# Kernel optimization log

Measured on AMD Instinct MI355X. Metric: run time of the kernel, lower is better.

The kernel has to match this reference:

```python
import jax, jax.numpy as jnp
import numpy as np

B_, L_, D_MODEL, N_LAYER, VOCAB = 4, 2048, 512, 2, 128
D_INNER, D_STATE, DT_RANK, D_CONV = 2 * D_MODEL, 16, D_MODEL // 16, 4
NDIR = 2  # forward / backward Mamba stacks


def setup_inputs() -> dict:
    key = jax.random.key(0)
    ks = jax.random.split(key, 12)
    f = jax.random.normal
    A_init = jnp.broadcast_to(
        jnp.log(jnp.arange(1, D_STATE + 1, dtype=jnp.float32)),
        (NDIR, N_LAYER, D_INNER, D_STATE)) + 0.0
    return {
        "input_ids": jax.random.randint(ks[0], (B_, L_), 0, VOCAB),
        "padding_mask": jnp.ones((B_, L_), dtype=bool),
        "embed": 0.02 * f(ks[1], (NDIR, VOCAB, D_MODEL)),
        "in_proj_w": 0.02 * f(ks[2], (NDIR, N_LAYER, 2 * D_INNER, D_MODEL)),
        "conv_w": 0.1 * f(ks[3], (NDIR, N_LAYER, D_INNER, 1, D_CONV)),
        "conv_b": 0.1 * f(ks[4], (NDIR, N_LAYER, D_INNER)),
        "x_proj_w": 0.02 * f(ks[5], (NDIR, N_LAYER, DT_RANK + 2 * D_STATE, D_INNER)),
        "dt_proj_w": 0.1 * f(ks[6], (NDIR, N_LAYER, D_INNER, DT_RANK)),
        "dt_proj_b": -4.0 + 0.5 * jax.random.uniform(ks[7], (NDIR, N_LAYER, D_INNER)),
        "A_log": A_init,
        "D": jnp.ones((NDIR, N_LAYER, D_INNER)),
        "out_proj_w": 0.02 * f(ks[8], (NDIR, N_LAYER, D_MODEL, D_INNER)),
        "norm_w": jnp.ones((NDIR, N_LAYER, D_MODEL)),
        "norm_f_w": jnp.ones((NDIR, D_MODEL)),
        "proj_w": 0.02 * f(ks[9], (D_MODEL, 2 * D_MODEL)),
        "proj_b": jnp.zeros((D_MODEL,)),
    }


def _rmsnorm(x, w, eps=1e-5):
    return x * jax.lax.rsqrt(jnp.mean(jnp.square(x), axis=-1, keepdims=True) + eps) * w


def _selective_scan(u, dt, Bm, Cm, A, Dp):
    # u, dt: (b, l, d_inner); Bm, Cm: (b, l, d_state)
    b, l, di = u.shape

    def step(h, inp):
        u_t, dt_t, b_t, c_t = inp                      # (b,di) (b,di) (b,n) (b,n)
        dA = jnp.exp(dt_t[:, :, None] * A)             # (b, di, n)
        h = dA * h + (dt_t * u_t)[:, :, None] * b_t[:, None, :]
        return h, jnp.einsum('bdn,bn->bd', h, c_t)

    h0 = jnp.zeros((b, di, A.shape[-1]), u.dtype)
    xs = (jnp.swapaxes(u, 0, 1), jnp.swapaxes(dt, 0, 1),
          jnp.swapaxes(Bm, 0, 1), jnp.swapaxes(Cm, 0, 1))
    _, ys = jax.lax.scan(step, h0, xs)                 # ys: (l, b, di)
    return jnp.swapaxes(ys, 0, 1) + u * Dp


def _mamba(x, p):
    in_w, cw, cb, xw, dtw, dtb, alog, dp, ow = p
    xz = jnp.einsum('bld,ed->ble', x, in_w)            # (b, l, 2*d_inner)
    u, z = jnp.split(xz, 2, axis=-1)
    uc = jnp.swapaxes(u, 1, 2)                         # (b, d_inner, l)
    uc = jax.lax.conv_general_dilated(
        uc, cw, (1,), [(D_CONV - 1, 0)], feature_group_count=D_INNER)
    u = jax.nn.silu(jnp.swapaxes(uc + cb[None, :, None], 1, 2))
    xdbl = jnp.einsum('bld,ed->ble', u, xw)
    dt, Bm, Cm = jnp.split(xdbl, [DT_RANK, DT_RANK + D_STATE], axis=-1)
    dt = jax.nn.softplus(jnp.einsum('blr,dr->bld', dt, dtw) + dtb)
    y = _selective_scan(u, dt, Bm, Cm, -jnp.exp(alog), dp)
    y = y * jax.nn.silu(z)
    return jnp.einsum('bld,ed->ble', y, ow)


def _mixer(ids, d, embed, in_proj_w, conv_w, conv_b, x_proj_w, dt_proj_w,
           dt_proj_b, A_log, D, out_proj_w, norm_w, norm_f_w):
    hidden = embed[d][ids]
    residual = None
    for i in range(N_LAYER):
        residual = hidden if residual is None else hidden + residual
        hidden = _rmsnorm(residual, norm_w[d, i])
        p = (in_proj_w[d, i], conv_w[d, i], conv_b[d, i], x_proj_w[d, i],
             dt_proj_w[d, i], dt_proj_b[d, i], A_log[d, i], D[d, i],
             out_proj_w[d, i])
        hidden = _mamba(hidden, p)
    return _rmsnorm(hidden + residual, norm_f_w[d])


def reference(input_ids, padding_mask, embed, in_proj_w, conv_w, conv_b,
              x_proj_w, dt_proj_w, dt_proj_b, A_log, D, out_proj_w, norm_w,
              norm_f_w, proj_w, proj_b):
    args = (embed, in_proj_w, conv_w, conv_b, x_proj_w, dt_proj_w, dt_proj_b,
            A_log, D, out_proj_w, norm_w, norm_f_w)
    fwd = _mixer(input_ids, 0, *args)
    bwd = jnp.flip(_mixer(jnp.flip(input_ids, 1), 1, *args), 1)
    out = jnp.concatenate([fwd, bwd], axis=-1)        # (b, l, 2*d_model)
    return jnp.einsum('ble,oe->blo', out, proj_w) + proj_b
```

## Files before the change

### kernel.cpp

```cpp
#include <hip/hip_runtime.h>
#include <hip/hip_bf16.h>

#define B_   4
#define L_   2048
#define DM   512
#define DI   1024
#define NST  16
#define DTR  32
#define ROWS (B_ * L_)
#define NCHUNK 64
#define CLEN  (L_ / NCHUNK)
#define LN2R 1.4426950408889634f

typedef unsigned short u16;
typedef __attribute__((ext_vector_type(8))) short bf16x8;
typedef __attribute__((ext_vector_type(4))) float f32x4;
typedef __attribute__((ext_vector_type(4))) float float4v;
typedef __attribute__((ext_vector_type(2))) float f32x2;

__device__ __forceinline__ float bf2f(u16 h) {
  union { unsigned int u; float f; } v; v.u = ((unsigned int)h) << 16; return v.f;
}
__device__ __forceinline__ u16 f2bf(float f) {
  union { float f; unsigned int u; } v; v.f = f;
  unsigned int u = v.u;
  if ((u & 0x7fffffffu) > 0x7f800000u) return (u16)((u >> 16) | 0x0040u);
  return (u16)((u + 0x7fffu + ((u >> 16) & 1u)) >> 16);
}
__device__ __forceinline__ float sigmoidf_(float x) { return 1.f / (1.f + __expf(-x)); }

__device__ __forceinline__ f32x2 pk_mul(f32x2 a, f32x2 b) {
  f32x2 d; asm("v_pk_mul_f32 %0, %1, %2" : "=v"(d) : "v"(a), "v"(b)); return d;
}
__device__ __forceinline__ f32x2 pk_fma(f32x2 a, f32x2 b, f32x2 c) {
  f32x2 d; asm("v_pk_fma_f32 %0, %1, %2, %3" : "=v"(d) : "v"(a), "v"(b), "v"(c)); return d;
}

__device__ __forceinline__ void gload16(const u16* g, u16* l) {
  __builtin_amdgcn_global_load_lds(
      (const __attribute__((address_space(1))) void*)g,
      (__attribute__((address_space(3))) void*)l, 16, 0, 0);
}

__global__ __launch_bounds__(256) void cvt_k(const float* __restrict__ in,
                                             u16* __restrict__ out, int n4) {
  int i = blockIdx.x * 256 + threadIdx.x;
  if (i >= n4) return;
  float4v v = *(const float4v*)&in[i * 4];
  u16 o[4];
  o[0] = f2bf(v.x); o[1] = f2bf(v.y); o[2] = f2bf(v.z); o[3] = f2bf(v.w);
  *(ulong1*)&out[i * 4] = *(ulong1*)o;
}

__global__ __launch_bounds__(256) void trp_k(const float* __restrict__ in,
                                             float* __restrict__ out) {
  int o = blockIdx.x * 256 + threadIdx.x;
  int li = o >> 15;
  int k = (o >> 10) & (DTR - 1);
  int d = o & (DI - 1);
  out[o] = in[((size_t)li * DI + d) * DTR + k];
}

__global__ __launch_bounds__(256) void embed_k(const int* __restrict__ ids,
                                               const float* __restrict__ emb,
                                               float* __restrict__ res, int flip) {
  int idx = blockIdx.x * 256 + threadIdx.x;
  int c = idx & (DM - 1);
  int row = idx >> 9;
  int b = row >> 11;
  int l = row & (L_ - 1);
  int sl = flip ? (L_ - 1 - l) : l;
  int id = ids[(b << 11) + sl];
  res[idx] = emb[id * DM + c];
}

template <bool ADD>
__global__ __launch_bounds__(256) void addnorm_k(float* __restrict__ res,
                                                 const float* __restrict__ hid,
                                                 const float* __restrict__ w,
                                                 u16* __restrict__ xn) {
  int row = blockIdx.x;
  int tid = threadIdx.x;
  int base = row * DM;
  float x0 = res[base + tid];
  float x1 = res[base + 256 + tid];
  if (ADD) {
    x0 += hid[base + tid];
    x1 += hid[base + 256 + tid];
    res[base + tid] = x0;
    res[base + 256 + tid] = x1;
  }
  float s = x0 * x0 + x1 * x1;
  for (int off = 32; off; off >>= 1) s += __shfl_xor(s, off);
  __shared__ float ps[4];
  if (!(tid & 63)) ps[tid >> 6] = s;
  __syncthreads();
  float tot = ps[0] + ps[1] + ps[2] + ps[3];
  float rs = 1.f / sqrtf(tot / (float)DM + 1e-5f);
  xn[base + tid]       = f2bf(x0 * rs * w[tid]);
  xn[base + 256 + tid] = f2bf(x1 * rs * w[tid + 256]);
}

#define EPI_F32  0
#define EPI_BF16 1
#define EPI_BIAS 2

template <int BN, int EPI, int SK = 1>
__global__ __launch_bounds__(256) void gemm_bt(const u16* __restrict__ A,
                                               const u16* __restrict__ W,
                                               void* __restrict__ outp,
                                               const float* __restrict__ bias,
                                               int N, int K) {
  constexpr int BM = 128, BK = 32;
  constexpr int NF = BN / 32;
  constexpr int G = (BN == 128) ? 4 : 3;
  __shared__ u16 As[4][BM * BK];
  __shared__ u16 Wsh[4][BN * BK];
  int tid = threadIdx.x;
  int lane = tid & 63;
  int wv = tid >> 6;
  int wr = wv >> 1, wc = wv & 1;
  int m0 = blockIdx.x * BM;
  int n0 = (SK > 1) ? 0 : blockIdx.y * BN;
  int koff = (SK > 1) ? blockIdx.y * (K / SK) : 0;
  int KS = K / SK;
  int NK = KS / BK;
  f32x4 acc[4][NF];
#pragma unroll
  for (int i = 0; i < 4; ++i)
#pragma unroll
    for (int j = 0; j < NF; ++j) acc[i][j] = (f32x4){0.f, 0.f, 0.f, 0.f};
  int rr = lane & 15;
  int kk = (lane >> 4) << 3;
  int l4 = lane >> 2;
  int c8 = (lane & 3) << 3;
  const u16* Ag = A + (size_t)(m0 + l4) * K + koff + c8;
  const u16* Wg = W + (size_t)(n0 + l4) * K + koff + c8;

  auto stage = [&](int k0, int buf) {
    gload16(Ag + (size_t)(wv * 16) * K + k0, &As[buf][wv * 512]);
    gload16(Ag + (size_t)((wv + 4) * 16) * K + k0, &As[buf][(wv + 4) * 512]);
    gload16(Wg + (size_t)(wv * 16) * K + k0, &Wsh[buf][wv * 512]);
    if (BN == 128)
      gload16(Wg + (size_t)((wv + 4) * 16) * K + k0, &Wsh[buf][(wv + 4) * 512]);
  };

  stage(0, 0); stage(BK, 1); stage(2 * BK, 2);
  for (int k = 0; k < NK; ++k) {
    if (k < NK - 2)
      asm volatile("s_waitcnt vmcnt(%0)" :: "n"(2 * G) : "memory");
    else if (k == NK - 2)
      asm volatile("s_waitcnt vmcnt(%0)" :: "n"(G) : "memory");
    else
      asm volatile("s_waitcnt vmcnt(0)" ::: "memory");
    __builtin_amdgcn_s_barrier();
    __builtin_amdgcn_sched_barrier(0);
    if (k + 3 < NK) stage((k + 3) * BK, (k + 3) & 3);
    __builtin_amdgcn_sched_barrier(0);
    int cur = k & 3;
    bf16x8 af[4], wf[NF];
#pragma unroll
    for (int mi = 0; mi < 4; ++mi)
      af[mi] = *(bf16x8*)&As[cur][(wr * 64 + mi * 16 + rr) * BK + kk];
#pragma unroll
    for (int ni = 0; ni < NF; ++ni)
      wf[ni] = *(bf16x8*)&Wsh[cur][(wc * (BN / 2) + ni * 16 + rr) * BK + kk];
#pragma unroll
    for (int mi = 0; mi < 4; ++mi)
#pragma unroll
      for (int ni = 0; ni < NF; ++ni)
        acc[mi][ni] = __builtin_amdgcn_mfma_f32_16x16x32_bf16(af[mi], wf[ni], acc[mi][ni], 0, 0, 0);
  }
  int cr = (lane >> 4) << 2;
  int cc = lane & 15;
  float* outF = (float*)outp + ((SK > 1) ? (size_t)blockIdx.y * (size_t)ROWS * N : 0);
#pragma unroll
  for (int mi = 0; mi < 4; ++mi)
#pragma unroll
    for (int ni = 0; ni < NF; ++ni) {
      int row = m0 + wr * 64 + mi * 16 + cr;
      int col = n0 + wc * (BN / 2) + ni * 16 + cc;
      float bv = (EPI == EPI_BIAS) ? bias[col] : 0.f;
#pragma unroll
      for (int j = 0; j < 4; ++j) {
        float v = acc[mi][ni][j] + bv;
        if (EPI == EPI_BF16)
          ((u16*)outp)[(size_t)(row + j) * N + col] = f2bf(v);
        else
          outF[(size_t)(row + j) * N + col] = v;
      }
    }
}

__global__ __launch_bounds__(256) void conv_k(const u16* __restrict__ xz,
                                              const float* __restrict__ cw,
                                              const float* __restrict__ cb,
                                              u16* __restrict__ uh) {
  int idx = blockIdx.x * 256 + threadIdx.x;
  int c = idx & (DI - 1);
  int row = idx >> 10;
  int l = row & (L_ - 1);
  float acc = cb[c];
#pragma unroll
  for (int j = 0; j < 4; ++j) {
    int ls = l + j - 3;
    if (ls >= 0)
      acc += bf2f(xz[(size_t)(row + j - 3) * (2 * DI) + c]) * cw[c * 4 + j];
  }
  float s = acc * sigmoidf_(acc);
  uh[idx] = f2bf(s);
}

__device__ __forceinline__ bool a_fast(const float* alog, int d, float& a20) {
  a20 = -__expf(alog[d * NST]) * LN2R;
  bool fast = true;
#pragma unroll
  for (int n = 1; n < NST; ++n) {
    float an = -__expf(alog[d * NST + n]) * LN2R;
    fast &= (fabsf(an - (float)(n + 1) * a20) <= 1e-5f * (float)(n + 1) * fabsf(a20));
  }
  return fast;
}

__device__ __forceinline__ void stage_xs(float (*xs)[64], const float* xp,
                                         int b, int t0, int tid) {
  size_t base = ((size_t)b * L_ + t0) * 64;
  const float4v* s0 = (const float4v*)(xp + base);
  const float4v* s1 = (const float4v*)(xp + (size_t)ROWS * 64 + base);
  const float4v* s2 = (const float4v*)(xp + (size_t)2 * ROWS * 64 + base);
  const float4v* s3 = (const float4v*)(xp + (size_t)3 * ROWS * 64 + base);
  float4v* dst = (float4v*)&xs[0][0];
  dst[tid]       = s0[tid]       + s1[tid]       + s2[tid]       + s3[tid];
  dst[tid + 256] = s0[tid + 256] + s1[tid + 256] + s2[tid + 256] + s3[tid + 256];
}

__global__ __launch_bounds__(256) void dtscan1_k(const u16* __restrict__ uh,
                                                 const float* __restrict__ xp,
                                                 const float* __restrict__ dtw_t,
                                                 const float* __restrict__ dtb,
                                                 const float* __restrict__ alog,
                                                 float* __restrict__ dtf,
                                                 float* __restrict__ chk) {
  __shared__ float xs[CLEN][64];
  int blk = blockIdx.x;
  int db = blk & 3;
  int c  = (blk >> 2) & (NCHUNK - 1);
  int b  = blk >> 8;
  int tid = threadIdx.x;
  int d  = db * 256 + tid;
  int t0 = c * CLEN;
  stage_xs(xs, xp, b, t0, tid);
  f32x2 w2[16];
#pragma unroll
  for (int j = 0; j < 16; ++j)
    w2[j] = (f32x2){dtw_t[(size_t)(2 * j) * DI + d], dtw_t[(size_t)(2 * j + 1) * DI + d]};
  float bias = dtb[d];
  float a20;
  bool fast = a_fast(alog, d, a20);
  __syncthreads();
  float S = 0.f;
  size_t ubase = ((size_t)b * L_ + t0) * DI + d;
  f32x2 h2[8];
#pragma unroll
  for (int q = 0; q < 8; ++q) h2[q] = (f32x2){0.f, 0.f};
  for (int t = 0; t < CLEN; ++t) {
    f32x2 a2 = {bias, 0.f};
    const f32x2* xr2 = (const f32x2*)&xs[t][0];
#pragma unroll
    for (int j = 0; j < 16; ++j) a2 = pk_fma(xr2[j], w2[j], a2);
    float a = a2.x + a2.y;
    float dtv = (a > 15.f) ? a : __logf(1.f + __expf(a));
    dtf[ubase] = dtv;
    float du = dtv * bf2f(uh[ubase]);
    S += dtv;
    if (fast) {
      float p1 = exp2f(dtv * a20);
      float p2 = p1 * p1;
      f32x2 pw = {p1, p2};
      f32x2 pst = {p2, p2};
      f32x2 du2 = {du, du};
#pragma unroll
      for (int k = 0; k < 4; ++k) {
        f32x4 bv = *(const f32x4*)&xs[t][DTR + k * 4];
        f32x2 blo = __builtin_shufflevector(bv, bv, 0, 1);
        f32x2 bhi = __builtin_shufflevector(bv, bv, 2, 3);
        h2[2 * k]     = pk_fma(pw, h2[2 * k], pk_mul(du2, blo));
        pw = pk_mul(pw, pst);
        h2[2 * k + 1] = pk_fma(pw, h2[2 * k + 1], pk_mul(du2, bhi));
        if (k < 3) pw = pk_mul(pw, pst);
      }
    } else {
#pragma unroll
      for (int q = 0; q < 8; ++q) {
        float e0 = exp2f(dtv * -__expf(alog[d * NST + 2 * q]) * LN2R);
        float e1 = exp2f(dtv * -__expf(alog[d * NST + 2 * q + 1]) * LN2R);
        f32x2 bv = *(const f32x2*)&xs[t][DTR + q * 2];
        h2[q] = pk_fma((f32x2){e0, e1}, h2[q], pk_mul((f32x2){du, du}, bv));
      }
    }
    ubase += DI;
  }
  const size_t H = (size_t)B_ * NCHUNK * DI * NST;
  size_t idx = ((size_t)(b * NCHUNK + c) * DI + d) * NST;
#pragma unroll
  for (int n = 0; n < NST; ++n) {
    float an = -__expf(alog[d * NST + n]) * LN2R;
    chk[idx + n]     = exp2f(an * S);
    chk[H + idx + n] = (n & 1) ? h2[n >> 1].y : h2[n >> 1].x;
  }
}

__global__ __launch_bounds__(256) void scan2_k(float* __restrict__ chk) {
  int j = blockIdx.x * 256 + threadIdx.x;
  int n = j & 15;
  int d = (j >> 4) & (DI - 1);
  int b = j >> 14;
  const size_t H = (size_t)B_ * NCHUNK * DI * NST;
  float h = 0.f;
  for (int c = 0; c < NCHUNK; ++c) {
    size_t idx = ((size_t)(b * NCHUNK + c) * DI + d) * NST + n;
    float a = chk[idx];
    float hl = chk[H + idx];
    chk[H + idx] = h;
    h = a * h + hl;
  }
}

__global__ __launch_bounds__(256) void scan3_k(const u16* __restrict__ uh,
                                               const float* __restrict__ dtf,
                                               const float* __restrict__ xp,
                                               const float* __restrict__ alog,
                                               const float* __restrict__ dvec,
                                               const float* __restrict__ chk,
                                               const u16* __restrict__ xz,
                                               u16* __restrict__ yg) {
  __shared__ float xs[CLEN][64];
  int blk = blockIdx.x;
  int db = blk & 3;
  int c  = (blk >> 2) & (NCHUNK - 1);
  int b  = blk >> 8;
  int tid = threadIdx.x;
  int d  = db * 256 + tid;
  int t0 = c * CLEN;
  stage_xs(xs, xp, b, t0, tid);
  float a20;
  bool fast = a_fast(alog, d, a20);
  const size_t H = (size_t)B_ * NCHUNK * DI * NST;
  size_t cidx = ((size_t)(b * NCHUNK + c) * DI + d) * NST;
  f32x2 h2[8];
#pragma unroll
  for (int q = 0; q < 8; ++q) h2[q] = *(const f32x2*)&chk[H + cidx + 2 * q];
  float Dv = dvec[d];
  __syncthreads();
  size_t ubase = ((size_t)b * L_ + t0) * DI + d;
  size_t zbase = ((size_t)b * L_ + t0) * (2 * DI) + DI + d;
  if (fast) {
    for (int t = 0; t < CLEN; ++t) {
      float dtv = dtf[ubase];
      float uv  = bf2f(uh[ubase]);
      float du  = dtv * uv;
      float p1 = exp2f(dtv * a20);
      float p2 = p1 * p1;
      f32x2 pw = {p1, p2};
      f32x2 pst = {p2, p2};
      f32x2 du2 = {du, du};
      f32x2 acc2 = {0.f, 0.f};
#pragma unroll
      for (int k = 0; k < 4; ++k) {
        f32x4 bv = *(const f32x4*)&xs[t][DTR + k * 4];
        f32x4 cv = *(const f32x4*)&xs[t][DTR + NST + k * 4];
        f32x2 blo = __builtin_shufflevector(bv, bv, 0, 1);
        f32x2 bhi = __builtin_shufflevector(bv, bv, 2, 3);
        f32x2 clo = __builtin_shufflevector(cv, cv, 0, 1);
        f32x2 chi = __builtin_shufflevector(cv, cv, 2, 3);
        h2[2 * k]     = pk_fma(pw, h2[2 * k], pk_mul(du2, blo));
        acc2          = pk_fma(h2[2 * k], clo, acc2);
        pw = pk_mul(pw, pst);
        h2[2 * k + 1] = pk_fma(pw, h2[2 * k + 1], pk_mul(du2, bhi));
        acc2          = pk_fma(h2[2 * k + 1], chi, acc2);
        if (k < 3) pw = pk_mul(pw, pst);
      }
      float y = acc2.x + acc2.y + uv * Dv;
      float z = bf2f(xz[zbase]);
      yg[ubase] = f2bf(y * z * sigmoidf_(z));
      ubase += DI; zbase += 2 * DI;
    }
  } else {
    float A2[NST];
#pragma unroll
    for (int n = 0; n < NST; ++n) A2[n] = -__expf(alog[d * NST + n]) * LN2R;
    for (int t = 0; t < CLEN; ++t) {
      float dtv = dtf[ubase];
      float uv  = bf2f(uh[ubase]);
      float du  = dtv * uv;
      f32x2 acc2 = {0.f, 0.f};
#pragma unroll
      for (int q = 0; q < 8; ++q) {
        f32x2 bv = *(const f32x2*)&xs[t][DTR + q * 2];
        f32x2 cv = *(const f32x2*)&xs[t][DTR + NST + q * 2];
        f32x2 e = {exp2f(dtv * A2[2 * q]), exp2f(dtv * A2[2 * q + 1])};
        h2[q] = pk_fma(e, h2[q], pk_mul((f32x2){du, du}, bv));
        acc2 = pk_fma(h2[q], cv, acc2);
      }
      float y = acc2.x + acc2.y + uv * Dv;
      float z = bf2f(xz[zbase]);
      yg[ubase] = f2bf(y * z * sigmoidf_(z));
      ubase += DI; zbase += 2 * DI;
    }
  }
}

__global__ __launch_bounds__(256) void fincat_k(const float* __restrict__ hid,
                                                const float* __restrict__ res,
                                                const float* __restrict__ w,
                                                u16* __restrict__ cat, int dir) {
  int row = blockIdx.x;
  int tid = threadIdx.x;
  int base = row * DM;
  float x0 = hid[base + tid] + res[base + tid];
  float x1 = hid[base + 256 + tid] + res[base + 256 + tid];
  float s = x0 * x0 + x1 * x1;
  for (int off = 32; off; off >>= 1) s += __shfl_xor(s, off);
  __shared__ float ps[4];
  if (!(tid & 63)) ps[tid >> 6] = s;
  __syncthreads();
  float tot = ps[0] + ps[1] + ps[2] + ps[3];
  float rs = 1.f / sqrtf(tot / (float)DM + 1e-5f);
  int b = row >> 11, l = row & (L_ - 1);
  size_t drow = dir ? ((size_t)(b << 11) + (L_ - 1 - l)) : (size_t)row;
  size_t obase = drow * (2 * DM) + (size_t)dir * DM;
  cat[obase + tid]       = f2bf(x0 * rs * w[tid]);
  cat[obase + 256 + tid] = f2bf(x1 * rs * w[tid + 256]);
}

extern "C" void kernel_launch(void* const* d_in, const int* in_sizes, int n_in,
                              void* d_out, int out_size, void* d_ws, size_t ws_size,
                              hipStream_t stream) {
  const int*   ids      = (const int*)d_in[0];
  const float* embed    = (const float*)d_in[2];
  const float* in_w     = (const float*)d_in[3];
  const float* conv_w   = (const float*)d_in[4];
  const float* conv_b   = (const float*)d_in[5];
  const float* x_w      = (const float*)d_in[6];
  const float* dt_w     = (const float*)d_in[7];
  const float* dt_bias  = (const float*)d_in[8];
  const float* A_log    = (const float*)d_in[9];
  const float* Dp       = (const float*)d_in[10];
  const float* out_w    = (const float*)d_in[11];
  const float* norm_w   = (const float*)d_in[12];
  const float* norm_f   = (const float*)d_in[13];
  const float* proj_w   = (const float*)d_in[14];
  const float* proj_b   = (const float*)d_in[15];

  char* ws = (char*)d_ws;
  size_t off = 0;
  auto alloc = [&](size_t bytes) {
    void* p = ws + off;
    off += (bytes + 255) & ~(size_t)255;
    return p;
  };
  float* res  = (float*)alloc((size_t)ROWS * DM * 4);
  float* hid  = (float*)alloc((size_t)ROWS * DM * 4);
  u16*   xnyg = (u16*)alloc((size_t)ROWS * DI * 2);
  u16*   xz   = (u16*)alloc((size_t)ROWS * 2 * DI * 2);
  u16*   u_h  = (u16*)alloc((size_t)ROWS * DI * 2);
  float* dtf  = (float*)alloc((size_t)ROWS * DI * 4);
  float* chk  = (float*)alloc((size_t)2 * B_ * NCHUNK * DI * NST * 4);
  u16*   cat  = (u16*)alloc((size_t)ROWS * 2 * DM * 2);
  const int N_IN  = 4 * 2 * DI * DM;
  const int N_XW  = 4 * 64 * DI;
  const int N_OW  = 4 * DM * DI;
  const int N_PW  = DM * 2 * DM;
  const int N_DTW = 4 * DTR * DI;
  u16*   in_wb  = (u16*)alloc((size_t)N_IN * 2);
  u16*   x_wb   = (u16*)alloc((size_t)N_XW * 2);
  u16*   out_wb = (u16*)alloc((size_t)N_OW * 2);
  u16*   pr_wb  = (u16*)alloc((size_t)N_PW * 2);
  float* dtw_t  = (float*)alloc((size_t)N_DTW * 4);
  if (off > ws_size) return;

  cvt_k<<<(N_IN / 4 + 255) / 256, 256, 0, stream>>>(in_w, in_wb, N_IN / 4);
  cvt_k<<<(N_XW / 4 + 255) / 256, 256, 0, stream>>>(x_w, x_wb, N_XW / 4);
  cvt_k<<<(N_OW / 4 + 255) / 256, 256, 0, stream>>>(out_w, out_wb, N_OW / 4);
  cvt_k<<<(N_PW / 4 + 255) / 256, 256, 0, stream>>>(proj_w, pr_wb, N_PW / 4);
  trp_k<<<N_DTW / 256, 256, 0, stream>>>(dt_w, dtw_t);

  for (int d = 0; d < 2; ++d) {
    embed_k<<<ROWS * DM / 256, 256, 0, stream>>>(ids, embed + (size_t)d * 128 * DM, res, d);
    for (int i = 0; i < 2; ++i) {
      int li = d * 2 + i;
      if (i == 0)
        addnorm_k<false><<<ROWS, 256, 0, stream>>>(res, hid, norm_w + (size_t)li * DM, xnyg);
      else
        addnorm_k<true><<<ROWS, 256, 0, stream>>>(res, hid, norm_w + (size_t)li * DM, xnyg);
      gemm_bt<128, EPI_BF16><<<dim3(ROWS / 128, 16), 256, 0, stream>>>(
          xnyg, in_wb + (size_t)li * 2 * DI * DM, xz, nullptr, 2 * DI, DM);
      conv_k<<<ROWS * DI / 256, 256, 0, stream>>>(
          xz, conv_w + (size_t)li * DI * 4, conv_b + (size_t)li * DI, u_h);
      gemm_bt<64, EPI_F32, 4><<<dim3(ROWS / 128, 4), 256, 0, stream>>>(
          u_h, x_wb + (size_t)li * 64 * DI, hid, nullptr, 64, DI);
      dtscan1_k<<<B_ * NCHUNK * (DI / 256), 256, 0, stream>>>(
          u_h, hid, dtw_t + (size_t)li * DTR * DI, dt_bias + (size_t)li * DI,
          A_log + (size_t)li * DI * NST, dtf, chk);
      scan2_k<<<(B_ * DI * NST) / 256, 256, 0, stream>>>(chk);
      scan3_k<<<B_ * NCHUNK * (DI / 256), 256, 0, stream>>>(
          u_h, dtf, hid, A_log + (size_t)li * DI * NST, Dp + (size_t)li * DI, chk,
          xz, xnyg);
      gemm_bt<64, EPI_F32><<<dim3(ROWS / 128, DM / 64), 256, 0, stream>>>(
          xnyg, out_wb + (size_t)li * DM * DI, hid, nullptr, DM, DI);
    }
    fincat_k<<<ROWS, 256, 0, stream>>>(hid, res, norm_f + (size_t)d * DM, cat, d);
  }
  gemm_bt<64, EPI_BIAS><<<dim3(ROWS / 128, DM / 64), 256, 0, stream>>>(
      cat, pr_wb, (float*)d_out, proj_b, DM, DI);
}
```

Measured before the change: 841.5 us.

## Use 256x256-tile GEMM with XCD-aware block mapping for in_proj

Replaces the 128-row tiled in_proj GEMM with a new kernel using 256x256 output tiles, 512 threads (8 waves each computing 128x64), and a 3-stage LDS pipeline. The block index is remapped so that blocks landing on the same XCD share A and W tiles, aiming for better L2 reuse. The larger tile raises arithmetic intensity per LDS load but uses heavy accumulator registers and gives only 256 blocks, which may limit occupancy. The epilogue writes bf16 with scattered 2-byte stores.

```diff
diff --git a/kernel.cpp b/kernel.cpp
--- a/kernel.cpp
+++ b/kernel.cpp
@@ -99,6 +99,80 @@
   float rs = 1.f / sqrtf(tot / (float)DM + 1e-5f);
   xn[base + tid]       = f2bf(x0 * rs * w[tid]);
   xn[base + 256 + tid] = f2bf(x1 * rs * w[tid + 256]);
+}
+
+__global__ __launch_bounds__(512) void gemm256_k(const u16* __restrict__ A,
+                                                 const u16* __restrict__ W,
+                                                 u16* __restrict__ outp,
+                                                 int N, int K) {
+  constexpr int BK = 32;
+  __shared__ u16 As[3][256 * BK];
+  __shared__ u16 Wsh[3][256 * BK];
+  int tid = threadIdx.x;
+  int lane = tid & 63;
+  int wv = tid >> 6;
+  int wr = wv >> 2, wc = wv & 3;
+  int bid = blockIdx.x;
+  int xcd = bid & 7, jj = bid >> 3;
+  int mt = (xcd & 3) * 8 + (jj & 7);
+  int nt = (xcd >> 2) * 4 + (jj >> 3);
+  int m0 = mt * 256, n0 = nt * 256;
+  f32x4 acc[8][4];
+#pragma unroll
+  for (int i = 0; i < 8; ++i)
+#pragma unroll
+    for (int j = 0; j < 4; ++j) acc[i][j] = (f32x4){0.f, 0.f, 0.f, 0.f};
+  int rr = lane & 15;
+  int kk = (lane >> 4) << 3;
+  int l4 = lane >> 2;
+  int c8 = (lane & 3) << 3;
+  const u16* Ag = A + (size_t)(m0 + l4) * K + c8;
+  const u16* Wg = W + (size_t)(n0 + l4) * K + c8;
+
+  auto stage = [&](int k0, int buf) {
+    gload16(Ag + (size_t)(wv * 16) * K + k0, &As[buf][wv * 512]);
+    gload16(Ag + (size_t)((wv + 8) * 16) * K + k0, &As[buf][(wv + 8) * 512]);
+    gload16(Wg + (size_t)(wv * 16) * K + k0, &Wsh[buf][wv * 512]);
+    gload16(Wg + (size_t)((wv + 8) * 16) * K + k0, &Wsh[buf][(wv + 8) * 512]);
+  };
+
+  int NK = K / BK;
+  stage(0, 0); stage(BK, 1);
+  for (int k = 0; k < NK; ++k) {
+    if (k < NK - 1)
+      asm volatile("s_waitcnt vmcnt(4)" ::: "memory");
+    else
+      asm volatile("s_waitcnt vmcnt(0)" ::: "memory");
+    __builtin_amdgcn_s_barrier();
+    __builtin_amdgcn_sched_barrier(0);
+    if (k + 2 < NK) stage((k + 2) * BK, (k + 2) % 3);
+    __builtin_amdgcn_sched_barrier(0);
+    int cur = k % 3;
+    bf16x8 af[8], wf[4];
+#pragma unroll
+    for (int mi = 0; mi < 8; ++mi)
+      af[mi] = *(bf16x8*)&As[cur][(wr * 128 + mi * 16 + rr) * BK + kk];
+#pragma unroll
+    for (int ni = 0; ni < 4; ++ni)
+      wf[ni] = *(bf16x8*)&Wsh[cur][(wc * 64 + ni * 16 + rr) * BK + kk];
+#pragma unroll
+    for (int mi = 0; mi < 8; ++mi)
+#pragma unroll
+      for (int ni = 0; ni < 4; ++ni)
+        acc[mi][ni] = __builtin_amdgcn_mfma_f32_16x16x32_bf16(af[mi], wf[ni], acc[mi][ni], 0, 0, 0);
+  }
+  int cr = (lane >> 4) << 2;
+  int cc = lane & 15;
+#pragma unroll
+  for (int mi = 0; mi < 8; ++mi)
+#pragma unroll
+    for (int ni = 0; ni < 4; ++ni) {
+      int row = m0 + wr * 128 + mi * 16 + cr;
+      int col = n0 + wc * 64 + ni * 16 + cc;
+#pragma unroll
+      for (int j = 0; j < 4; ++j)
+        outp[(size_t)(row + j) * N + col] = f2bf(acc[mi][ni][j]);
+    }
 }
 
 #define EPI_F32  0
@@ -493,8 +567,8 @@
         addnorm_k<false><<<ROWS, 256, 0, stream>>>(res, hid, norm_w + (size_t)li * DM, xnyg);
       else
         addnorm_k<true><<<ROWS, 256, 0, stream>>>(res, hid, norm_w + (size_t)li * DM, xnyg);
-      gemm_bt<128, EPI_BF16><<<dim3(ROWS / 128, 16), 256, 0, stream>>>(
-          xnyg, in_wb + (size_t)li * 2 * DI * DM, xz, nullptr, 2 * DI, DM);
+      gemm256_k<<<256, 512, 0, stream>>>(
+          xnyg, in_wb + (size_t)li * 2 * DI * DM, xz, 2 * DI, DM);
       conv_k<<<ROWS * DI / 256, 256, 0, stream>>>(
           xz, conv_w + (size_t)li * DI * 4, conv_b + (size_t)li * DI, u_h);
       gemm_bt<64, EPI_F32, 4><<<dim3(ROWS / 128, 4), 256, 0, stream>>>(
```

Result: no change. 842.7 us (+0.2%).
